# Optimization experiments

Hardware: AMD Instinct MI355X
Metric: run time of the kernel (lower is better)

The kernel has to match this reference:

```python
import jax, jax.numpy as jnp
import numpy as np

N, D, K = 65536, 512, 4096


def setup_inputs() -> dict:
    key = jax.random.key(0)
    kx, kc = jax.random.split(key)
    x = jax.random.normal(kx, (N, D), dtype=jnp.float32)
    center = jax.random.normal(kc, (K, D), dtype=jnp.float32)
    return {"x": x, "center": center}


def squared_euclidean(x, center):
    x_sq = jnp.sum(x * x, axis=1, keepdims=True)        # [N,1]
    c_sq = jnp.sum(center * center, axis=1)             # [K]
    cross = x @ center.T                                # [N,K] GEMM
    return x_sq - 2.0 * cross + c_sq[None, :]


def reference(x, center):
    # KMeans.forward: dis_func(input, center).argmin(1)
    dist = squared_euclidean(x, center)                 # [N,K]
    return jnp.argmin(dist, axis=1)                     # [N] int32
```

## Files before the change

### kernel.cpp

```cpp
#include <hip/hip_runtime.h>

#define N_ROWS 65536
#define DIM    512
#define K_CENT 4096
#define TILE_M 128
#define TILE_N 128
#define BK     64
#define KSTEPS (DIM / BK)
#define NKT    (K_CENT / TILE_N)
#define THREADS 512
#define MARGIN 22.0f
#define CAND_CAP 1536
#define COMPACT_TRIG 1024
#define SCALE1 0x7F7F7F7F

typedef float  floatx4  __attribute__((ext_vector_type(4)));
typedef float  floatx16 __attribute__((ext_vector_type(16)));
typedef int    intx2    __attribute__((ext_vector_type(2)));
typedef int    intx4    __attribute__((ext_vector_type(4)));
typedef int    intx8    __attribute__((ext_vector_type(8)));

__device__ __forceinline__ unsigned mapF(float f) {
  unsigned u = __float_as_uint(f);
  return (u & 0x80000000u) ? ~u : (u | 0x80000000u);
}
__device__ __forceinline__ float unmapF(unsigned m) {
  unsigned u = (m & 0x80000000u) ? (m ^ 0x80000000u) : ~m;
  return __uint_as_float(u);
}

__device__ __forceinline__ void gload_lds16(const void* g, void* l) {
  __builtin_amdgcn_global_load_lds(
      (const __attribute__((address_space(1))) void*)g,
      (__attribute__((address_space(3))) void*)l, 16, 0, 0);
}

__device__ __forceinline__ int pk4(float a, float b, float c, float d) {
  int r = __builtin_amdgcn_cvt_pk_fp8_f32(a, b, 0, false);
  r = __builtin_amdgcn_cvt_pk_fp8_f32(c, d, r, true);
  return r;
}

__global__ void prep_convert(const float* __restrict__ x, const float* __restrict__ c,
                             unsigned char* __restrict__ xq, unsigned char* __restrict__ cq,
                             float* __restrict__ csqg) {
  const size_t nx = (size_t)N_ROWS * DIM;
  size_t i = ((size_t)blockIdx.x * blockDim.x + threadIdx.x) * 8;
  if (i < nx) {
    floatx4 a = *(const floatx4*)(x + i);
    floatx4 b = *(const floatx4*)(x + i + 4);
    intx2 q = { pk4(a[0], a[1], a[2], a[3]), pk4(b[0], b[1], b[2], b[3]) };
    *(intx2*)(xq + i) = q;
  } else if (i < nx + (size_t)K_CENT * DIM) {
    size_t off = i - nx;
    floatx4 a = *(const floatx4*)(c + off);
    floatx4 b = *(const floatx4*)(c + off + 4);
    intx2 q = { pk4(a[0], a[1], a[2], a[3]), pk4(b[0], b[1], b[2], b[3]) };
    *(intx2*)(cq + off) = q;
    float s = a[0]*a[0]+a[1]*a[1]+a[2]*a[2]+a[3]*a[3]
            + b[0]*b[0]+b[1]*b[1]+b[2]*b[2]+b[3]*b[3];
#pragma unroll
    for (int o = 1; o < 64; o <<= 1) s += __shfl_xor(s, o, 64);
    if ((threadIdx.x & 63) == 0) csqg[off >> 9] = s;
  }
}

template <int MODE>
__global__ __launch_bounds__(THREADS, 4)
void kmeans_argmin(const float* __restrict__ x, const float* __restrict__ cent,
                   const unsigned char* __restrict__ xq, const unsigned char* __restrict__ cq,
                   const float* __restrict__ csqg, int* __restrict__ out) {
  __shared__ unsigned char ldsA[TILE_M * BK];
  __shared__ unsigned char ldsB[TILE_N * BK];
  __shared__ float csq4[TILE_N][4];
  __shared__ unsigned sminU[TILE_M];
  __shared__ unsigned long long best[TILE_M];
  __shared__ unsigned candKey[CAND_CAP];
  __shared__ float candS[CAND_CAP];
  __shared__ int candCount;

  const int t = threadIdx.x;
  const int lane = t & 63;
  const int wave = t >> 6;
  const int wm = wave >> 1;
  const int wn = wave & 1;
  const int l31 = lane & 31;
  const int half = lane >> 5;
  const int rowBlock = blockIdx.x * TILE_M;

  if (t < TILE_M) { sminU[t] = 0xFFFFFFFFu; best[t] = ~0ull; }
  if (t == 0) candCount = 0;

  const int rS = (t >> 2) & 31;
  const int rowS = (t >> 7) * 32 + rS;
  const int offS = (((t & 3) ^ ((rS >> 1) & 3)) << 4);

  const int qk = half * 2;
  const int fragSlotBase = 4 * l31 + (qk ^ ((l31 >> 1) & 3));

  for (int kt = 0; kt < NKT; ++kt) {
    const int ktBase = kt * TILE_N;
    if (MODE == 0) ((float*)csq4)[t] = 0.f;
    floatx16 acc[2];
#pragma unroll
    for (int fn = 0; fn < 2; ++fn)
#pragma unroll
      for (int e = 0; e < 16; ++e) acc[fn][e] = 0.f;

    for (int ks = 0; ks < KSTEPS; ++ks) {
      const int kd = ks * BK;
      if (MODE == 2) {
        gload_lds16(xq + (size_t)(rowBlock + rowS) * DIM + kd + offS,
                    ldsA + (size_t)wave * 1024);
        gload_lds16(cq + (size_t)(ktBase + rowS) * DIM + kd + offS,
                    ldsB + (size_t)wave * 1024);
      } else {
        {
          const float* gA = x + (size_t)(rowBlock + rowS) * DIM + kd + offS;
          floatx4 f0 = *(const floatx4*)gA, f1 = *(const floatx4*)(gA + 4);
          floatx4 f2 = *(const floatx4*)(gA + 8), f3 = *(const floatx4*)(gA + 12);
          intx4 q = { pk4(f0[0],f0[1],f0[2],f0[3]), pk4(f1[0],f1[1],f1[2],f1[3]),
                      pk4(f2[0],f2[1],f2[2],f2[3]), pk4(f3[0],f3[1],f3[2],f3[3]) };
          *(intx4*)(ldsA + (size_t)t * 16) = q;
        }
        {
          const float* gB = cent + (size_t)(ktBase + rowS) * DIM + kd + offS;
          floatx4 f0 = *(const floatx4*)gB, f1 = *(const floatx4*)(gB + 4);
          floatx4 f2 = *(const floatx4*)(gB + 8), f3 = *(const floatx4*)(gB + 12);
          intx4 q = { pk4(f0[0],f0[1],f0[2],f0[3]), pk4(f1[0],f1[1],f1[2],f1[3]),
                      pk4(f2[0],f2[1],f2[2],f2[3]), pk4(f3[0],f3[1],f3[2],f3[3]) };
          *(intx4*)(ldsB + (size_t)t * 16) = q;
          float s = 0.f;
#pragma unroll
          for (int e = 0; e < 4; ++e)
            s += f0[e]*f0[e] + f1[e]*f1[e] + f2[e]*f2[e] + f3[e]*f3[e];
          csq4[rowS][t & 3] += s;
        }
      }
      __syncthreads();

      intx8 aF, bF[2];
      {
        int s0 = wm * 128 + fragSlotBase;
        intx4 lo = *(const intx4*)(ldsA + s0 * 16);
        intx4 hi = *(const intx4*)(ldsA + (s0 ^ 1) * 16);
        aF = (intx8){lo[0], lo[1], lo[2], lo[3], hi[0], hi[1], hi[2], hi[3]};
      }
#pragma unroll
      for (int fn = 0; fn < 2; ++fn) {
        int s0 = (wn * 2 + fn) * 128 + fragSlotBase;
        intx4 lo = *(const intx4*)(ldsB + s0 * 16);
        intx4 hi = *(const intx4*)(ldsB + (s0 ^ 1) * 16);
        bF[fn] = (intx8){lo[0], lo[1], lo[2], lo[3], hi[0], hi[1], hi[2], hi[3]};
      }
#pragma unroll
      for (int fn = 0; fn < 2; ++fn)
        acc[fn] = __builtin_amdgcn_mfma_scale_f32_32x32x64_f8f6f4(
            aF, bF[fn], acc[fn], 0, 0, 0, SCALE1, 0, SCALE1);
      __syncthreads();
    }

    float cs[2];
#pragma unroll
    for (int fn = 0; fn < 2; ++fn) {
      int cl = wn * 64 + fn * 32 + l31;
      cs[fn] = (MODE == 2) ? csqg[ktBase + cl]
                           : (csq4[cl][0] + csq4[cl][1] + csq4[cl][2] + csq4[cl][3]);
    }

#pragma unroll
    for (int r = 0; r < 16; ++r) {
      float v = fminf(cs[0] - 2.f * acc[0][r], cs[1] - 2.f * acc[1][r]);
      v = fminf(v, __shfl_xor(v, 1, 64));
      v = fminf(v, __shfl_xor(v, 2, 64));
      v = fminf(v, __shfl_xor(v, 4, 64));
      v = fminf(v, __shfl_xor(v, 8, 64));
      v = fminf(v, __shfl_xor(v, 16, 64));
      if (l31 == 0) {
        int srow = wm * 32 + (r & 3) + 8 * (r >> 2) + 4 * half;
        atomicMin(&sminU[srow], mapF(v));
      }
    }
    __syncthreads();

#pragma unroll
    for (int r = 0; r < 16; ++r) {
      int srow = wm * 32 + (r & 3) + 8 * (r >> 2) + 4 * half;
      float thr = unmapF(sminU[srow]) + MARGIN;
#pragma unroll
      for (int fn = 0; fn < 2; ++fn) {
        float s = cs[fn] - 2.f * acc[fn][r];
        if (s <= thr) {
          int k = ktBase + wn * 64 + fn * 32 + l31;
          int idx = atomicAdd(&candCount, 1);
          if (idx < CAND_CAP) {
            candKey[idx] = ((unsigned)k << 7) | (unsigned)srow;
            candS[idx] = s;
          }
        }
      }
    }
    __syncthreads();

    if (candCount > COMPACT_TRIG) {
      int cc = candCount; if (cc > CAND_CAP) cc = CAND_CAP;
      unsigned myK[4]; float myS[4]; int myN = 0;
      for (int i = t; i < cc; i += THREADS) {
        int rl = candKey[i] & 127;
        if (candS[i] <= unmapF(sminU[rl]) + MARGIN && myN < 4) {
          myK[myN] = candKey[i]; myS[myN] = candS[i]; ++myN;
        }
      }
      __syncthreads();
      if (t == 0) candCount = 0;
      __syncthreads();
      int base = atomicAdd(&candCount, myN);
      for (int j = 0; j < myN; ++j) { candKey[base + j] = myK[j]; candS[base + j] = myS[j]; }
      __syncthreads();
    }
  }

  int cnt = candCount; if (cnt > CAND_CAP) cnt = CAND_CAP;
  const int g = t >> 4;
  const int sl = t & 15;
  for (int ci = g; ci < cnt; ci += 32) {
    unsigned cd = candKey[ci];
    int rl = cd & 127;
    if (candS[ci] > unmapF(sminU[rl]) + MARGIN) continue;
    int k = cd >> 7;
    const float* xr = x + (size_t)(rowBlock + rl) * DIM;
    const float* cr = cent + (size_t)k * DIM;
    double d = 0.0;
#pragma unroll
    for (int j = 0; j < DIM / 64; ++j) {
      floatx4 xv = *(const floatx4*)(xr + j * 64 + sl * 4);
      floatx4 cv = *(const floatx4*)(cr + j * 64 + sl * 4);
#pragma unroll
      for (int e = 0; e < 4; ++e) {
        double df = (double)xv[e] - (double)cv[e];
        d += df * df;
      }
    }
#pragma unroll
    for (int off = 1; off < 16; off <<= 1) d += __shfl_xor(d, off, 64);
    if (sl == 0) {
      unsigned long long key =
          ((unsigned long long)__double_as_longlong(d) & ~0xFFFull) | (unsigned long long)k;
      atomicMin(&best[rl], key);
    }
  }
  __syncthreads();
  if (t < TILE_M) out[rowBlock + t] = (int)(best[t] & 0xFFFull);
}

extern "C" void kernel_launch(void* const* d_in, const int* in_sizes, int n_in,
                              void* d_out, int out_size, void* d_ws, size_t ws_size,
                              hipStream_t stream) {
  const float* x = (const float*)d_in[0];
  const float* cent = (const float*)d_in[1];
  int* out = (int*)d_out;
  const size_t nXq = (size_t)N_ROWS * DIM;
  const size_t nCq = (size_t)K_CENT * DIM;
  const size_t nCsq = (size_t)K_CENT * sizeof(float);
  const int grid = N_ROWS / TILE_M;

  if (ws_size >= nXq + nCq + nCsq) {
    unsigned char* xq = (unsigned char*)d_ws;
    unsigned char* cq = xq + nXq;
    float* csqg = (float*)(cq + nCq);
    const size_t total8 = ((size_t)N_ROWS + K_CENT) * DIM / 8;
    prep_convert<<<(unsigned)((total8 + 255) / 256), 256, 0, stream>>>(x, cent, xq, cq, csqg);
    kmeans_argmin<2><<<grid, THREADS, 0, stream>>>(x, cent, xq, cq, csqg, out);
  } else {
    kmeans_argmin<0><<<grid, THREADS, 0, stream>>>(x, cent, nullptr, nullptr, nullptr, out);
  }
}
```

Baseline: 626.3 us.

## Triple-buffer fp8 LDS tiles with async prefetch across flattened k-loop

The fp8 path becomes a flattened loop over all centroid tiles and k-steps. Global-to-LDS loads run two steps ahead into a three-buffer ring, using explicit vmcnt waits and raw barriers in place of two __syncthreads per step. Centroid norms are staged once into LDS, and the prep kernel converts 16 elements per thread instead of 8. This uses about 48KB of dynamic LDS plus a 16KB norm table and lowers the occupancy hint from 4 to 2, which could cut latency hiding.

```diff
diff --git a/kernel.cpp b/kernel.cpp
--- a/kernel.cpp
+++ b/kernel.cpp
@@ -8,6 +8,7 @@
 #define BK     64
 #define KSTEPS (DIM / BK)
 #define NKT    (K_CENT / TILE_N)
+#define NSTEP  (NKT * KSTEPS)
 #define THREADS 512
 #define MARGIN 22.0f
 #define CAND_CAP 1536
@@ -41,38 +42,50 @@
   return r;
 }
 
+#define FENCE_BAR() do { asm volatile("s_waitcnt lgkmcnt(0)" ::: "memory"); \
+                         __builtin_amdgcn_s_barrier();                       \
+                         __builtin_amdgcn_sched_barrier(0); } while (0)
+
 __global__ void prep_convert(const float* __restrict__ x, const float* __restrict__ c,
                              unsigned char* __restrict__ xq, unsigned char* __restrict__ cq,
                              float* __restrict__ csqg) {
   const size_t nx = (size_t)N_ROWS * DIM;
-  size_t i = ((size_t)blockIdx.x * blockDim.x + threadIdx.x) * 8;
+  size_t i = ((size_t)blockIdx.x * blockDim.x + threadIdx.x) * 16;
   if (i < nx) {
-    floatx4 a = *(const floatx4*)(x + i);
-    floatx4 b = *(const floatx4*)(x + i + 4);
-    intx2 q = { pk4(a[0], a[1], a[2], a[3]), pk4(b[0], b[1], b[2], b[3]) };
-    *(intx2*)(xq + i) = q;
+    floatx4 a0 = *(const floatx4*)(x + i);
+    floatx4 a1 = *(const floatx4*)(x + i + 4);
+    floatx4 a2 = *(const floatx4*)(x + i + 8);
+    floatx4 a3 = *(const floatx4*)(x + i + 12);
+    intx4 q = { pk4(a0[0],a0[1],a0[2],a0[3]), pk4(a1[0],a1[1],a1[2],a1[3]),
+                pk4(a2[0],a2[1],a2[2],a2[3]), pk4(a3[0],a3[1],a3[2],a3[3]) };
+    *(intx4*)(xq + i) = q;
   } else if (i < nx + (size_t)K_CENT * DIM) {
     size_t off = i - nx;
-    floatx4 a = *(const floatx4*)(c + off);
-    floatx4 b = *(const floatx4*)(c + off + 4);
-    intx2 q = { pk4(a[0], a[1], a[2], a[3]), pk4(b[0], b[1], b[2], b[3]) };
-    *(intx2*)(cq + off) = q;
-    float s = a[0]*a[0]+a[1]*a[1]+a[2]*a[2]+a[3]*a[3]
-            + b[0]*b[0]+b[1]*b[1]+b[2]*b[2]+b[3]*b[3];
-#pragma unroll
-    for (int o = 1; o < 64; o <<= 1) s += __shfl_xor(s, o, 64);
-    if ((threadIdx.x & 63) == 0) csqg[off >> 9] = s;
-  }
-}
-
-template <int MODE>
-__global__ __launch_bounds__(THREADS, 4)
-void kmeans_argmin(const float* __restrict__ x, const float* __restrict__ cent,
-                   const unsigned char* __restrict__ xq, const unsigned char* __restrict__ cq,
-                   const float* __restrict__ csqg, int* __restrict__ out) {
-  __shared__ unsigned char ldsA[TILE_M * BK];
-  __shared__ unsigned char ldsB[TILE_N * BK];
-  __shared__ float csq4[TILE_N][4];
+    floatx4 a0 = *(const floatx4*)(c + off);
+    floatx4 a1 = *(const floatx4*)(c + off + 4);
+    floatx4 a2 = *(const floatx4*)(c + off + 8);
+    floatx4 a3 = *(const floatx4*)(c + off + 12);
+    intx4 q = { pk4(a0[0],a0[1],a0[2],a0[3]), pk4(a1[0],a1[1],a1[2],a1[3]),
+                pk4(a2[0],a2[1],a2[2],a2[3]), pk4(a3[0],a3[1],a3[2],a3[3]) };
+    *(intx4*)(cq + off) = q;
+    float s = 0.f;
+#pragma unroll
+    for (int e = 0; e < 4; ++e)
+      s += a0[e]*a0[e] + a1[e]*a1[e] + a2[e]*a2[e] + a3[e]*a3[e];
+#pragma unroll
+    for (int o = 1; o < 32; o <<= 1) s += __shfl_xor(s, o, 64);
+    if ((threadIdx.x & 31) == 0) csqg[off >> 9] = s;
+  }
+}
+
+__global__ __launch_bounds__(THREADS, 2)
+void kmeans_argmin_pipe(const float* __restrict__ x, const float* __restrict__ cent,
+                        const unsigned char* __restrict__ xq, const unsigned char* __restrict__ cq,
+                        const float* __restrict__ csqg, int* __restrict__ out) {
+  extern __shared__ __align__(16) unsigned char dynLds[];
+  unsigned char* ldsA = dynLds;
+  unsigned char* ldsB = dynLds + 3 * 8192;
+  __shared__ float csqL[K_CENT];
   __shared__ unsigned sminU[TILE_M];
   __shared__ unsigned long long best[TILE_M];
   __shared__ unsigned candKey[CAND_CAP];
@@ -90,135 +103,141 @@
 
   if (t < TILE_M) { sminU[t] = 0xFFFFFFFFu; best[t] = ~0ull; }
   if (t == 0) candCount = 0;
+  for (int i = t; i < K_CENT; i += THREADS) csqL[i] = csqg[i];
 
   const int rS = (t >> 2) & 31;
   const int rowS = (t >> 7) * 32 + rS;
   const int offS = (((t & 3) ^ ((rS >> 1) & 3)) << 4);
-
   const int qk = half * 2;
   const int fragSlotBase = 4 * l31 + (qk ^ ((l31 >> 1) & 3));
 
-  for (int kt = 0; kt < NKT; ++kt) {
-    const int ktBase = kt * TILE_N;
-    if (MODE == 0) ((float*)csq4)[t] = 0.f;
-    floatx16 acc[2];
+  const size_t aRowOff = (size_t)(rowBlock + rowS) * DIM + offS;
+
+  asm volatile("s_waitcnt vmcnt(0)" ::: "memory");
+  gload_lds16(xq + aRowOff + 0,  ldsA + wave * 1024);
+  gload_lds16(cq + (size_t)rowS * DIM + 0 + offS,  ldsB + wave * 1024);
+  gload_lds16(xq + aRowOff + 64, ldsA + 8192 + wave * 1024);
+  gload_lds16(cq + (size_t)rowS * DIM + 64 + offS, ldsB + 8192 + wave * 1024);
+  FENCE_BAR();
+
+  floatx16 acc[2];
+#pragma unroll
+  for (int fn = 0; fn < 2; ++fn)
+#pragma unroll
+    for (int e = 0; e < 16; ++e) acc[fn][e] = 0.f;
+
+  int bi = 0;
+  for (int j = 0; j < NSTEP; ++j) {
+    const int kt = j >> 3, ks = j & 7;
+    if (j + 2 < NSTEP) {
+      const int j2 = j + 2;
+      const int kt2 = j2 >> 3, ks2 = j2 & 7;
+      int b2 = bi + 2; if (b2 >= 3) b2 -= 3;
+      gload_lds16(xq + aRowOff + (ks2 << 6), ldsA + (b2 << 13) + wave * 1024);
+      gload_lds16(cq + (size_t)((kt2 << 7) + rowS) * DIM + (ks2 << 6) + offS,
+                  ldsB + (b2 << 13) + wave * 1024);
+      asm volatile("s_waitcnt vmcnt(4)" ::: "memory");
+    } else if (j + 2 == NSTEP) {
+      asm volatile("s_waitcnt vmcnt(2)" ::: "memory");
+    } else {
+      asm volatile("s_waitcnt vmcnt(0)" ::: "memory");
+    }
+    __builtin_amdgcn_s_barrier();
+    __builtin_amdgcn_sched_barrier(0);
+
+    const unsigned char* A = ldsA + (bi << 13);
+    const unsigned char* B = ldsB + (bi << 13);
+    intx8 aF, bF[2];
+    {
+      int s0 = wm * 128 + fragSlotBase;
+      intx4 lo = *(const intx4*)(A + s0 * 16);
+      intx4 hi = *(const intx4*)(A + (s0 ^ 1) * 16);
+      aF = (intx8){lo[0], lo[1], lo[2], lo[3], hi[0], hi[1], hi[2], hi[3]};
+    }
+#pragma unroll
+    for (int fn = 0; fn < 2; ++fn) {
+      int s0 = (wn * 2 + fn) * 128 + fragSlotBase;
+      intx4 lo = *(const intx4*)(B + s0 * 16);
+      intx4 hi = *(const intx4*)(B + (s0 ^ 1) * 16);
+      bF[fn] = (intx8){lo[0], lo[1], lo[2], lo[3], hi[0], hi[1], hi[2], hi[3]};
+    }
+    asm volatile("s_waitcnt lgkmcnt(0)" ::: "memory");
+    __builtin_amdgcn_sched_barrier(0);
 #pragma unroll
     for (int fn = 0; fn < 2; ++fn)
-#pragma unroll
-      for (int e = 0; e < 16; ++e) acc[fn][e] = 0.f;
-
-    for (int ks = 0; ks < KSTEPS; ++ks) {
-      const int kd = ks * BK;
-      if (MODE == 2) {
-        gload_lds16(xq + (size_t)(rowBlock + rowS) * DIM + kd + offS,
-                    ldsA + (size_t)wave * 1024);
-        gload_lds16(cq + (size_t)(ktBase + rowS) * DIM + kd + offS,
-                    ldsB + (size_t)wave * 1024);
-      } else {
-        {
-          const float* gA = x + (size_t)(rowBlock + rowS) * DIM + kd + offS;
-          floatx4 f0 = *(const floatx4*)gA, f1 = *(const floatx4*)(gA + 4);
-          floatx4 f2 = *(const floatx4*)(gA + 8), f3 = *(const floatx4*)(gA + 12);
-          intx4 q = { pk4(f0[0],f0[1],f0[2],f0[3]), pk4(f1[0],f1[1],f1[2],f1[3]),
-                      pk4(f2[0],f2[1],f2[2],f2[3]), pk4(f3[0],f3[1],f3[2],f3[3]) };
-          *(intx4*)(ldsA + (size_t)t * 16) = q;
+      acc[fn] = __builtin_amdgcn_mfma_scale_f32_32x32x64_f8f6f4(
+          aF, bF[fn], acc[fn], 0, 0, 0, SCALE1, 0, SCALE1);
+
+    if (ks == KSTEPS - 1) {
+      const int ktBase = kt << 7;
+      float cs[2];
+#pragma unroll
+      for (int fn = 0; fn < 2; ++fn)
+        cs[fn] = csqL[ktBase + wn * 64 + fn * 32 + l31];
+
+#pragma unroll
+      for (int r = 0; r < 16; ++r) {
+        float v = fminf(cs[0] - 2.f * acc[0][r], cs[1] - 2.f * acc[1][r]);
+        v = fminf(v, __shfl_xor(v, 1, 64));
+        v = fminf(v, __shfl_xor(v, 2, 64));
+        v = fminf(v, __shfl_xor(v, 4, 64));
+        v = fminf(v, __shfl_xor(v, 8, 64));
+        v = fminf(v, __shfl_xor(v, 16, 64));
+        if (l31 == 0) {
+          int srow = wm * 32 + (r & 3) + 8 * (r >> 2) + 4 * half;
+          atomicMin(&sminU[srow], mapF(v));
         }
-        {
-          const float* gB = cent + (size_t)(ktBase + rowS) * DIM + kd + offS;
-          floatx4 f0 = *(const floatx4*)gB, f1 = *(const floatx4*)(gB + 4);
-          floatx4 f2 = *(const floatx4*)(gB + 8), f3 = *(const floatx4*)(gB + 12);
-          intx4 q = { pk4(f0[0],f0[1],f0[2],f0[3]), pk4(f1[0],f1[1],f1[2],f1[3]),
-                      pk4(f2[0],f2[1],f2[2],f2[3]), pk4(f3[0],f3[1],f3[2],f3[3]) };
-          *(intx4*)(ldsB + (size_t)t * 16) = q;
-          float s = 0.f;
-#pragma unroll
-          for (int e = 0; e < 4; ++e)
-            s += f0[e]*f0[e] + f1[e]*f1[e] + f2[e]*f2[e] + f3[e]*f3[e];
-          csq4[rowS][t & 3] += s;
-        }
-      }
-      __syncthreads();
-
-      intx8 aF, bF[2];
-      {
-        int s0 = wm * 128 + fragSlotBase;
-        intx4 lo = *(const intx4*)(ldsA + s0 * 16);
-        intx4 hi = *(const intx4*)(ldsA + (s0 ^ 1) * 16);
-        aF = (intx8){lo[0], lo[1], lo[2], lo[3], hi[0], hi[1], hi[2], hi[3]};
-      }
-#pragma unroll
-      for (int fn = 0; fn < 2; ++fn) {
-        int s0 = (wn * 2 + fn) * 128 + fragSlotBase;
-        intx4 lo = *(const intx4*)(ldsB + s0 * 16);
-        intx4 hi = *(const intx4*)(ldsB + (s0 ^ 1) * 16);
-        bF[fn] = (intx8){lo[0], lo[1], lo[2], lo[3], hi[0], hi[1], hi[2], hi[3]};
-      }
-#pragma unroll
-      for (int fn = 0; fn < 2; ++fn)
-        acc[fn] = __builtin_amdgcn_mfma_scale_f32_32x32x64_f8f6f4(
-            aF, bF[fn], acc[fn], 0, 0, 0, SCALE1, 0, SCALE1);
-      __syncthreads();
-    }
-
-    float cs[2];
-#pragma unroll
-    for (int fn = 0; fn < 2; ++fn) {
-      int cl = wn * 64 + fn * 32 + l31;
-      cs[fn] = (MODE == 2) ? csqg[ktBase + cl]
-                           : (csq4[cl][0] + csq4[cl][1] + csq4[cl][2] + csq4[cl][3]);
-    }
-
-#pragma unroll
-    for (int r = 0; r < 16; ++r) {
-      float v = fminf(cs[0] - 2.f * acc[0][r], cs[1] - 2.f * acc[1][r]);
-      v = fminf(v, __shfl_xor(v, 1, 64));
-      v = fminf(v, __shfl_xor(v, 2, 64));
-      v = fminf(v, __shfl_xor(v, 4, 64));
-      v = fminf(v, __shfl_xor(v, 8, 64));
-      v = fminf(v, __shfl_xor(v, 16, 64));
-      if (l31 == 0) {
+      }
+      FENCE_BAR();
+
+#pragma unroll
+      for (int r = 0; r < 16; ++r) {
         int srow = wm * 32 + (r & 3) + 8 * (r >> 2) + 4 * half;
-        atomicMin(&sminU[srow], mapF(v));
-      }
-    }
-    __syncthreads();
-
-#pragma unroll
-    for (int r = 0; r < 16; ++r) {
-      int srow = wm * 32 + (r & 3) + 8 * (r >> 2) + 4 * half;
-      float thr = unmapF(sminU[srow]) + MARGIN;
-#pragma unroll
-      for (int fn = 0; fn < 2; ++fn) {
-        float s = cs[fn] - 2.f * acc[fn][r];
-        if (s <= thr) {
-          int k = ktBase + wn * 64 + fn * 32 + l31;
-          int idx = atomicAdd(&candCount, 1);
-          if (idx < CAND_CAP) {
-            candKey[idx] = ((unsigned)k << 7) | (unsigned)srow;
-            candS[idx] = s;
+        float thr = unmapF(sminU[srow]) + MARGIN;
+#pragma unroll
+        for (int fn = 0; fn < 2; ++fn) {
+          float s = cs[fn] - 2.f * acc[fn][r];
+          if (s <= thr) {
+            int k = ktBase + wn * 64 + fn * 32 + l31;
+            int idx = atomicAdd(&candCount, 1);
+            if (idx < CAND_CAP) {
+              candKey[idx] = ((unsigned)k << 7) | (unsigned)srow;
+              candS[idx] = s;
+            }
           }
         }
       }
-    }
-    __syncthreads();
-
-    if (candCount > COMPACT_TRIG) {
-      int cc = candCount; if (cc > CAND_CAP) cc = CAND_CAP;
-      unsigned myK[4]; float myS[4]; int myN = 0;
-      for (int i = t; i < cc; i += THREADS) {
-        int rl = candKey[i] & 127;
-        if (candS[i] <= unmapF(sminU[rl]) + MARGIN && myN < 4) {
-          myK[myN] = candKey[i]; myS[myN] = candS[i]; ++myN;
+      FENCE_BAR();
+
+      if (candCount > COMPACT_TRIG) {
+        int cc = candCount; if (cc > CAND_CAP) cc = CAND_CAP;
+        unsigned myK[4]; float myS[4]; int myN = 0;
+        for (int i = t; i < cc; i += THREADS) {
+          int rl = candKey[i] & 127;
+          if (candS[i] <= unmapF(sminU[rl]) + MARGIN && myN < 4) {
+            myK[myN] = candKey[i]; myS[myN] = candS[i]; ++myN;
+          }
         }
-      }
-      __syncthreads();
-      if (t == 0) candCount = 0;
-      __syncthreads();
-      int base = atomicAdd(&candCount, myN);
-      for (int j = 0; j < myN; ++j) { candKey[base + j] = myK[j]; candS[base + j] = myS[j]; }
-      __syncthreads();
-    }
-  }
+        FENCE_BAR();
+        if (t == 0) candCount = 0;
+        FENCE_BAR();
+        int base = atomicAdd(&candCount, myN);
+        for (int jj = 0; jj < myN; ++jj) { candKey[base + jj] = myK[jj]; candS[base + jj] = myS[jj]; }
+        FENCE_BAR();
+      }
+
+#pragma unroll
+      for (int fn = 0; fn < 2; ++fn)
+#pragma unroll
+        for (int e = 0; e < 16; ++e) acc[fn][e] = 0.f;
+    } else {
+      __builtin_amdgcn_s_barrier();
+      __builtin_amdgcn_sched_barrier(0);
+    }
+    ++bi; if (bi == 3) bi = 0;
+  }
+
+  __syncthreads();
 
   int cnt = candCount; if (cnt > CAND_CAP) cnt = CAND_CAP;
   const int g = t >> 4;
@@ -232,6 +251,183 @@
     const float* cr = cent + (size_t)k * DIM;
     double d = 0.0;
 #pragma unroll
+    for (int jj = 0; jj < DIM / 64; ++jj) {
+      floatx4 xv = *(const floatx4*)(xr + jj * 64 + sl * 4);
+      floatx4 cv = *(const floatx4*)(cr + jj * 64 + sl * 4);
+#pragma unroll
+      for (int e = 0; e < 4; ++e) {
+        double df = (double)xv[e] - (double)cv[e];
+        d += df * df;
+      }
+    }
+#pragma unroll
+    for (int off = 1; off < 16; off <<= 1) d += __shfl_xor(d, off, 64);
+    if (sl == 0) {
+      unsigned long long key =
+          ((unsigned long long)__double_as_longlong(d) & ~0xFFFull) | (unsigned long long)k;
+      atomicMin(&best[rl], key);
+    }
+  }
+  __syncthreads();
+  if (t < TILE_M) out[rowBlock + t] = (int)(best[t] & 0xFFFull);
+}
+
+__global__ __launch_bounds__(THREADS, 4)
+void kmeans_argmin_fb(const float* __restrict__ x, const float* __restrict__ cent,
+                      int* __restrict__ out) {
+  __shared__ unsigned char ldsA[TILE_M * BK];
+  __shared__ unsigned char ldsB[TILE_N * BK];
+  __shared__ float csq4[TILE_N][4];
+  __shared__ unsigned sminU[TILE_M];
+  __shared__ unsigned long long best[TILE_M];
+  __shared__ unsigned candKey[CAND_CAP];
+  __shared__ float candS[CAND_CAP];
+  __shared__ int candCount;
+
+  const int t = threadIdx.x;
+  const int lane = t & 63;
+  const int wave = t >> 6;
+  const int wm = wave >> 1;
+  const int wn = wave & 1;
+  const int l31 = lane & 31;
+  const int half = lane >> 5;
+  const int rowBlock = blockIdx.x * TILE_M;
+
+  if (t < TILE_M) { sminU[t] = 0xFFFFFFFFu; best[t] = ~0ull; }
+  if (t == 0) candCount = 0;
+
+  const int rS = (t >> 2) & 31;
+  const int rowS = (t >> 7) * 32 + rS;
+  const int offS = (((t & 3) ^ ((rS >> 1) & 3)) << 4);
+  const int qk = half * 2;
+  const int fragSlotBase = 4 * l31 + (qk ^ ((l31 >> 1) & 3));
+
+  for (int kt = 0; kt < NKT; ++kt) {
+    const int ktBase = kt * TILE_N;
+    ((float*)csq4)[t] = 0.f;
+    floatx16 acc[2];
+#pragma unroll
+    for (int fn = 0; fn < 2; ++fn)
+#pragma unroll
+      for (int e = 0; e < 16; ++e) acc[fn][e] = 0.f;
+
+    for (int ks = 0; ks < KSTEPS; ++ks) {
+      const int kd = ks * BK;
+      {
+        const float* gA = x + (size_t)(rowBlock + rowS) * DIM + kd + offS;
+        floatx4 f0 = *(const floatx4*)gA, f1 = *(const floatx4*)(gA + 4);
+        floatx4 f2 = *(const floatx4*)(gA + 8), f3 = *(const floatx4*)(gA + 12);
+        intx4 q = { pk4(f0[0],f0[1],f0[2],f0[3]), pk4(f1[0],f1[1],f1[2],f1[3]),
+                    pk4(f2[0],f2[1],f2[2],f2[3]), pk4(f3[0],f3[1],f3[2],f3[3]) };
+        *(intx4*)(ldsA + (size_t)t * 16) = q;
+      }
+      {
+        const float* gB = cent + (size_t)(ktBase + rowS) * DIM + kd + offS;
+        floatx4 f0 = *(const floatx4*)gB, f1 = *(const floatx4*)(gB + 4);
+        floatx4 f2 = *(const floatx4*)(gB + 8), f3 = *(const floatx4*)(gB + 12);
+        intx4 q = { pk4(f0[0],f0[1],f0[2],f0[3]), pk4(f1[0],f1[1],f1[2],f1[3]),
+                    pk4(f2[0],f2[1],f2[2],f2[3]), pk4(f3[0],f3[1],f3[2],f3[3]) };
+        *(intx4*)(ldsB + (size_t)t * 16) = q;
+        float s = 0.f;
+#pragma unroll
+        for (int e = 0; e < 4; ++e)
+          s += f0[e]*f0[e] + f1[e]*f1[e] + f2[e]*f2[e] + f3[e]*f3[e];
+        csq4[rowS][t & 3] += s;
+      }
+      __syncthreads();
+
+      intx8 aF, bF[2];
+      {
+        int s0 = wm * 128 + fragSlotBase;
+        intx4 lo = *(const intx4*)(ldsA + s0 * 16);
+        intx4 hi = *(const intx4*)(ldsA + (s0 ^ 1) * 16);
+        aF = (intx8){lo[0], lo[1], lo[2], lo[3], hi[0], hi[1], hi[2], hi[3]};
+      }
+#pragma unroll
+      for (int fn = 0; fn < 2; ++fn) {
+        int s0 = (wn * 2 + fn) * 128 + fragSlotBase;
+        intx4 lo = *(const intx4*)(ldsB + s0 * 16);
+        intx4 hi = *(const intx4*)(ldsB + (s0 ^ 1) * 16);
+        bF[fn] = (intx8){lo[0], lo[1], lo[2], lo[3], hi[0], hi[1], hi[2], hi[3]};
+      }
+#pragma unroll
+      for (int fn = 0; fn < 2; ++fn)
+        acc[fn] = __builtin_amdgcn_mfma_scale_f32_32x32x64_f8f6f4(
+            aF, bF[fn], acc[fn], 0, 0, 0, SCALE1, 0, SCALE1);
+      __syncthreads();
+    }
+
+    float cs[2];
+#pragma unroll
+    for (int fn = 0; fn < 2; ++fn) {
+      int cl = wn * 64 + fn * 32 + l31;
+      cs[fn] = csq4[cl][0] + csq4[cl][1] + csq4[cl][2] + csq4[cl][3];
+    }
+
+#pragma unroll
+    for (int r = 0; r < 16; ++r) {
+      float v = fminf(cs[0] - 2.f * acc[0][r], cs[1] - 2.f * acc[1][r]);
+      v = fminf(v, __shfl_xor(v, 1, 64));
+      v = fminf(v, __shfl_xor(v, 2, 64));
+      v = fminf(v, __shfl_xor(v, 4, 64));
+      v = fminf(v, __shfl_xor(v, 8, 64));
+      v = fminf(v, __shfl_xor(v, 16, 64));
+      if (l31 == 0) {
+        int srow = wm * 32 + (r & 3) + 8 * (r >> 2) + 4 * half;
+        atomicMin(&sminU[srow], mapF(v));
+      }
+    }
+    __syncthreads();
+
+#pragma unroll
+    for (int r = 0; r < 16; ++r) {
+      int srow = wm * 32 + (r & 3) + 8 * (r >> 2) + 4 * half;
+      float thr = unmapF(sminU[srow]) + MARGIN;
+#pragma unroll
+      for (int fn = 0; fn < 2; ++fn) {
+        float s = cs[fn] - 2.f * acc[fn][r];
+        if (s <= thr) {
+          int k = ktBase + wn * 64 + fn * 32 + l31;
+          int idx = atomicAdd(&candCount, 1);
+          if (idx < CAND_CAP) {
+            candKey[idx] = ((unsigned)k << 7) | (unsigned)srow;
+            candS[idx] = s;
+          }
+        }
+      }
+    }
+    __syncthreads();
+
+    if (candCount > COMPACT_TRIG) {
+      int cc = candCount; if (cc > CAND_CAP) cc = CAND_CAP;
+      unsigned myK[4]; float myS[4]; int myN = 0;
+      for (int i = t; i < cc; i += THREADS) {
+        int rl = candKey[i] & 127;
+        if (candS[i] <= unmapF(sminU[rl]) + MARGIN && myN < 4) {
+          myK[myN] = candKey[i]; myS[myN] = candS[i]; ++myN;
+        }
+      }
+      __syncthreads();
+      if (t == 0) candCount = 0;
+      __syncthreads();
+      int base = atomicAdd(&candCount, myN);
+      for (int j = 0; j < myN; ++j) { candKey[base + j] = myK[j]; candS[base + j] = myS[j]; }
+      __syncthreads();
+    }
+  }
+
+  int cnt = candCount; if (cnt > CAND_CAP) cnt = CAND_CAP;
+  const int g = t >> 4;
+  const int sl = t & 15;
+  for (int ci = g; ci < cnt; ci += 32) {
+    unsigned cd = candKey[ci];
+    int rl = cd & 127;
+    if (candS[ci] > unmapF(sminU[rl]) + MARGIN) continue;
+    int k = cd >> 7;
+    const float* xr = x + (size_t)(rowBlock + rl) * DIM;
+    const float* cr = cent + (size_t)k * DIM;
+    double d = 0.0;
+#pragma unroll
     for (int j = 0; j < DIM / 64; ++j) {
       floatx4 xv = *(const floatx4*)(xr + j * 64 + sl * 4);
       floatx4 cv = *(const floatx4*)(cr + j * 64 + sl * 4);
@@ -268,10 +464,10 @@
     unsigned char* xq = (unsigned char*)d_ws;
     unsigned char* cq = xq + nXq;
     float* csqg = (float*)(cq + nCq);
-    const size_t total8 = ((size_t)N_ROWS + K_CENT) * DIM / 8;
-    prep_convert<<<(unsigned)((total8 + 255) / 256), 256, 0, stream>>>(x, cent, xq, cq, csqg);
-    kmeans_argmin<2><<<grid, THREADS, 0, stream>>>(x, cent, xq, cq, csqg, out);
+    const size_t total16 = ((size_t)N_ROWS + K_CENT) * DIM / 16;
+    prep_convert<<<(unsigned)((total16 + 255) / 256), 256, 0, stream>>>(x, cent, xq, cq, csqg);
+    kmeans_argmin_pipe<<<grid, THREADS, 6 * 8192, stream>>>(x, cent, xq, cq, csqg, out);
   } else {
-    kmeans_argmin<0><<<grid, THREADS, 0, stream>>>(x, cent, nullptr, nullptr, nullptr, out);
-  }
-}
+    kmeans_argmin_fb<<<grid, THREADS, 0, stream>>>(x, cent, out);
+  }
+}
```

After: 623.6 us. About the same (-0.4%).
